# Optimization experiments

Measured on AMD Instinct MI355X. Metric: run time of the kernel, lower is better.

The kernel has to match this reference:

```python
import jax, jax.numpy as jnp
import numpy as np

EPS = 1e-6
N_HEADS = 16
N_KV_HEADS = 4
HEAD_DIM = 128
DIM = 2048
SEQ = 2048
BATCH = 2


def _make_freqs_cis(seqlen, head_dim, theta=10000.0):
    inv = 1.0 / (theta ** (jnp.arange(0, head_dim, 2, dtype=jnp.float32) / head_dim))  # [hd/2]
    t = jnp.arange(seqlen, dtype=jnp.float32)
    ang = jnp.outer(t, inv)  # [seq, hd/2]
    return jnp.stack([jnp.cos(ang), jnp.sin(ang)], axis=-1)  # [seq, hd/2, 2]


def setup_inputs() -> dict:
    key = jax.random.key(0)
    k1, k2, k3 = jax.random.split(key, 3)
    std = 0.02
    x = jax.random.normal(k1, (BATCH, SEQ, DIM), dtype=jnp.float32)
    freqs_cis = _make_freqs_cis(SEQ, HEAD_DIM)
    norm_w = jnp.ones((DIM,), dtype=jnp.float32)
    wqkv_w = jax.random.normal(k2, ((N_HEADS + 2 * N_KV_HEADS) * HEAD_DIM, DIM), dtype=jnp.float32) * std
    wo_w = jax.random.normal(k3, (DIM, N_HEADS * HEAD_DIM), dtype=jnp.float32) * std
    return {"x": x, "freqs_cis": freqs_cis, "norm_w": norm_w, "wqkv_w": wqkv_w, "wo_w": wo_w}


def _rope(t, cos, sin):
    # t: [b, s, h, hd] viewed as pairs; cos/sin: [s, hd/2]
    b, s, h, hd = t.shape
    tr = t.reshape(b, s, h, hd // 2, 2)
    xr, xi = tr[..., 0], tr[..., 1]
    c = cos[None, :, None, :]
    sn = sin[None, :, None, :]
    out_r = xr * c - xi * sn
    out_i = xr * sn + xi * c
    return jnp.stack([out_r, out_i], axis=-1).reshape(b, s, h, hd)


def reference(x, freqs_cis, norm_w, wqkv_w, wo_w):
    bs, seqlen, dim = x.shape
    n_rep = N_HEADS // N_KV_HEADS
    # RMSNorm
    xn = x * jax.lax.rsqrt(jnp.mean(x * x, axis=-1, keepdims=True) + EPS) * norm_w
    # fused QKV projection
    qkv = jnp.einsum('bsd,ed->bse', xn, wqkv_w)
    q_sz = N_HEADS * HEAD_DIM
    kv_sz = N_KV_HEADS * HEAD_DIM
    xq = qkv[..., :q_sz].reshape(bs, seqlen, N_HEADS, HEAD_DIM)
    xk = qkv[..., q_sz:q_sz + kv_sz].reshape(bs, seqlen, N_KV_HEADS, HEAD_DIM)
    xv = qkv[..., q_sz + kv_sz:].reshape(bs, seqlen, N_KV_HEADS, HEAD_DIM)
    cos, sin = freqs_cis[..., 0], freqs_cis[..., 1]
    xq = _rope(xq, cos, sin)
    xk = _rope(xk, cos, sin)
    # GQA: group q heads so kv broadcast replaces repeat_kv materialization
    q = xq.transpose(0, 2, 1, 3).reshape(bs, N_KV_HEADS, n_rep, seqlen, HEAD_DIM)
    k = xk.transpose(0, 2, 1, 3)  # [b, g, s, d]
    v = xv.transpose(0, 2, 1, 3)
    scale = 1.0 / jnp.sqrt(jnp.float32(HEAD_DIM))
    scores = jnp.einsum('bgrqd,bgkd->bgrqk', q, k) * scale
    causal = jnp.tril(jnp.ones((seqlen, seqlen), dtype=bool))
    scores = jnp.where(causal, scores, jnp.finfo(scores.dtype).min)
    probs = jax.nn.softmax(scores, axis=-1)
    out = jnp.einsum('bgrqk,bgkd->bgrqd', probs, v)
    out = out.reshape(bs, N_HEADS, seqlen, HEAD_DIM).transpose(0, 2, 1, 3).reshape(bs, seqlen, N_HEADS * HEAD_DIM)
    return jnp.einsum('bse,de->bsd', out, wo_w)
```

## Files before the change

### kernel.cpp

```cpp
#include <hip/hip_runtime.h>
#include <cstdint>
#include <cstddef>

typedef __bf16 bhalf;
typedef __bf16 bhalf8 __attribute__((ext_vector_type(8)));
typedef __bf16 bhalf4 __attribute__((ext_vector_type(4)));
typedef float f32x4 __attribute__((ext_vector_type(4)));
typedef float f32x16 __attribute__((ext_vector_type(16)));

#define RMS_EPS 1e-6f
#define N_HEADS 16
#define N_KV 4
#define HD 128
#define DIM 2048
#define SEQ 2048
#define BATCH 2

static __device__ __forceinline__ f32x4 mfma16(bhalf8 a, bhalf8 b, f32x4 c) {
    return __builtin_amdgcn_mfma_f32_16x16x32_bf16(a, b, c, 0, 0, 0);
}
static __device__ __forceinline__ f32x16 mfma32(bhalf8 a, bhalf8 b, f32x16 c) {
    return __builtin_amdgcn_mfma_f32_32x32x16_bf16(a, b, c, 0, 0, 0);
}

static __device__ __forceinline__ void gload16(const bhalf* g, bhalf* l) {
    __builtin_amdgcn_global_load_lds((const __attribute__((address_space(1))) unsigned int*)g,
                                     (__attribute__((address_space(3))) unsigned int*)l,
                                     16, 0, 0);
}

__global__ __launch_bounds__(256) void cvt_w(const float* __restrict__ a,
                                             const float* __restrict__ b,
                                             bhalf* __restrict__ dst) {
    size_t i = ((size_t)blockIdx.x * 256 + threadIdx.x) * 4;
    const size_t NQ = (size_t)3072 * 2048;
    float4 v = (i < NQ) ? ((const float4*)a)[i >> 2] : ((const float4*)b)[(i - NQ) >> 2];
    bhalf4 o;
    o[0] = (bhalf)v.x; o[1] = (bhalf)v.y; o[2] = (bhalf)v.z; o[3] = (bhalf)v.w;
    *(bhalf4*)(dst + i) = o;
}

__global__ __launch_bounds__(256) void rmsnorm_k(const float* __restrict__ x,
                                                 const float* __restrict__ w,
                                                 bhalf* __restrict__ xn) {
    const int row = blockIdx.x;
    const int tid = threadIdx.x;
    const float4* xr = (const float4*)(x + (size_t)row * DIM);
    float4 v0 = xr[tid * 2], v1 = xr[tid * 2 + 1];
    float ss = v0.x * v0.x + v0.y * v0.y + v0.z * v0.z + v0.w * v0.w
             + v1.x * v1.x + v1.y * v1.y + v1.z * v1.z + v1.w * v1.w;
    #pragma unroll
    for (int off = 32; off; off >>= 1) ss += __shfl_xor(ss, off, 64);
    __shared__ float red[4];
    if ((tid & 63) == 0) red[tid >> 6] = ss;
    __syncthreads();
    float tot = red[0] + red[1] + red[2] + red[3];
    float scale = rsqrtf(tot * (1.0f / DIM) + RMS_EPS);
    const float4* wr = (const float4*)w;
    float4 w0 = wr[tid * 2], w1 = wr[tid * 2 + 1];
    bhalf8 o;
    o[0] = (bhalf)(v0.x * scale * w0.x); o[1] = (bhalf)(v0.y * scale * w0.y);
    o[2] = (bhalf)(v0.z * scale * w0.z); o[3] = (bhalf)(v0.w * scale * w0.w);
    o[4] = (bhalf)(v1.x * scale * w1.x); o[5] = (bhalf)(v1.y * scale * w1.y);
    o[6] = (bhalf)(v1.z * scale * w1.z); o[7] = (bhalf)(v1.w * scale * w1.w);
    *(bhalf8*)(xn + (size_t)row * DIM + tid * 8) = o;
}

template <typename OutT>
__global__ __launch_bounds__(256) void gemm_abt(const bhalf* __restrict__ A,
                                                const bhalf* __restrict__ B,
                                                OutT* __restrict__ C,
                                                int N, int K) {
    const int tid = threadIdx.x;
    const int wave = tid >> 6, lane = tid & 63;
    const int quad = lane >> 4, r16 = lane & 15;
    const int m0 = blockIdx.y * 128, n0 = blockIdx.x * 128;
    const int wm = (wave >> 1) * 64, wn = (wave & 1) * 64;

    __shared__ __align__(16) bhalf sA[128][32];
    __shared__ __align__(16) bhalf sB[128][32];

    f32x4 acc[4][4];
    #pragma unroll
    for (int i = 0; i < 4; ++i)
        #pragma unroll
        for (int j = 0; j < 4; ++j) acc[i][j] = (f32x4)0.0f;

    const int lrow = lane >> 2;
    const int lcol = (lane & 3) * 8;
    const int arow = 32 * wave + lrow;
    const bhalf* Ap = A + (size_t)(m0 + arow) * K + lcol;
    const bhalf* Bp = B + (size_t)(n0 + arow) * K + lcol;
    const size_t rs16 = (size_t)16 * K;
    bhalf* sAp0 = &sA[32 * wave][0];
    bhalf* sAp1 = &sA[32 * wave + 16][0];
    bhalf* sBp0 = &sB[32 * wave][0];
    bhalf* sBp1 = &sB[32 * wave + 16][0];

    for (int k0 = 0; k0 < K; k0 += 32) {
        __syncthreads();
        gload16(Ap + k0, sAp0);
        gload16(Ap + k0 + rs16, sAp1);
        gload16(Bp + k0, sBp0);
        gload16(Bp + k0 + rs16, sBp1);
        __syncthreads();
        bhalf8 af[4], bfr[4];
        #pragma unroll
        for (int i = 0; i < 4; ++i) af[i]  = *(bhalf8*)&sA[wm + i * 16 + r16][quad * 8];
        #pragma unroll
        for (int j = 0; j < 4; ++j) bfr[j] = *(bhalf8*)&sB[wn + j * 16 + r16][quad * 8];
        #pragma unroll
        for (int i = 0; i < 4; ++i)
            #pragma unroll
            for (int j = 0; j < 4; ++j)
                acc[i][j] = mfma16(af[i], bfr[j], acc[i][j]);
    }

    #pragma unroll
    for (int i = 0; i < 4; ++i) {
        const int rbase = m0 + wm + i * 16 + quad * 4;
        #pragma unroll
        for (int rr = 0; rr < 4; ++rr) {
            OutT* crow = C + (size_t)(rbase + rr) * N + n0 + wn + r16;
            #pragma unroll
            for (int j = 0; j < 4; ++j) crow[j * 16] = (OutT)acc[i][j][rr];
        }
    }
}

__global__ __launch_bounds__(256) void rope_k(const bhalf* __restrict__ qkv,
                                              const float* __restrict__ freqs,
                                              bhalf* __restrict__ qb,
                                              bhalf* __restrict__ kb,
                                              bhalf* __restrict__ vt) {
    const int bs = blockIdx.x;
    const int b = bs >> 11, s = bs & 2047;
    const bhalf* row = qkv + (size_t)bs * 3072;
    const int tid = threadIdx.x;

    {
        const int h = tid >> 4, d20 = (tid & 15) * 4;
        bhalf8 e = *(const bhalf8*)(row + h * HD + d20 * 2);
        const float* fp = freqs + (size_t)s * 128 + d20 * 2;
        float4 f0 = *(const float4*)fp;
        float4 f1 = *(const float4*)(fp + 4);
        bhalf8 o;
        o[0] = (bhalf)((float)e[0] * f0.x - (float)e[1] * f0.y);
        o[1] = (bhalf)((float)e[0] * f0.y + (float)e[1] * f0.x);
        o[2] = (bhalf)((float)e[2] * f0.z - (float)e[3] * f0.w);
        o[3] = (bhalf)((float)e[2] * f0.w + (float)e[3] * f0.z);
        o[4] = (bhalf)((float)e[4] * f1.x - (float)e[5] * f1.y);
        o[5] = (bhalf)((float)e[4] * f1.y + (float)e[5] * f1.x);
        o[6] = (bhalf)((float)e[6] * f1.z - (float)e[7] * f1.w);
        o[7] = (bhalf)((float)e[6] * f1.w + (float)e[7] * f1.z);
        *(bhalf8*)(qb + ((size_t)(b * N_HEADS + h) * SEQ + s) * HD + d20 * 2) = o;
    }
    if (tid < 64) {
        const int kh = tid >> 4, d20 = (tid & 15) * 4;
        bhalf8 e = *(const bhalf8*)(row + 2048 + kh * HD + d20 * 2);
        const float* fp = freqs + (size_t)s * 128 + d20 * 2;
        float4 f0 = *(const float4*)fp;
        float4 f1 = *(const float4*)(fp + 4);
        bhalf8 o;
        o[0] = (bhalf)((float)e[0] * f0.x - (float)e[1] * f0.y);
        o[1] = (bhalf)((float)e[0] * f0.y + (float)e[1] * f0.x);
        o[2] = (bhalf)((float)e[2] * f0.z - (float)e[3] * f0.w);
        o[3] = (bhalf)((float)e[2] * f0.w + (float)e[3] * f0.z);
        o[4] = (bhalf)((float)e[4] * f1.x - (float)e[5] * f1.y);
        o[5] = (bhalf)((float)e[4] * f1.y + (float)e[5] * f1.x);
        o[6] = (bhalf)((float)e[6] * f1.z - (float)e[7] * f1.w);
        o[7] = (bhalf)((float)e[6] * f1.w + (float)e[7] * f1.z);
        *(bhalf8*)(kb + ((size_t)(b * N_KV + kh) * SEQ + s) * HD + d20 * 2) = o;
    }
    for (int e = tid; e < 512; e += 256) {
        const int kh = e >> 7, d = e & 127;
        vt[((size_t)(b * N_KV + kh) * HD + d) * SEQ + s] = row[2560 + e];
    }
}

__global__ __launch_bounds__(256, 1) void attn_k(const bhalf* __restrict__ qb,
                                                 const bhalf* __restrict__ kb,
                                                 const bhalf* __restrict__ vt,
                                                 bhalf* __restrict__ ob) {
    const int tid = threadIdx.x;
    const int wave = tid >> 6, lane = tid & 63;
    const int l31 = lane & 31, h2 = lane >> 5;
    const int pair = blockIdx.x & 7;
    const int hh = (blockIdx.x >> 3) & 15;
    const int b = blockIdx.x >> 7;
    const int kvh = hh >> 2;

    __shared__ __align__(16) bhalf sK[64][136];
    __shared__ __align__(16) bhalf sV[128][72];
    __shared__ __align__(16) bhalf sP[4][32][72];

    const bhalf* Kbase = kb + (size_t)(b * N_KV + kvh) * SEQ * HD;
    const bhalf* Vbase = vt + (size_t)(b * N_KV + kvh) * HD * SEQ;
    const float SCL2 = 0.08838834764831845f * 1.4426950408889634f;

    const int kr = tid >> 4, kc = (tid & 15) * 8;
    const int vr = tid >> 3, vc = (tid & 7) * 8;

    for (int phase = 0; phase < 2; ++phase) {
        const int qt = phase ? (15 - pair) : pair;
        const int ktmax = 2 * qt + 1;
        const int qrow = qt * 128 + wave * 32 + l31;

        const bhalf* qbase = qb + (((size_t)(b * N_HEADS + hh) * SEQ) + qrow) * HD;
        bhalf8 qf[8];
        #pragma unroll
        for (int kk = 0; kk < 8; ++kk) {
            bhalf8 q0 = *(const bhalf8*)(qbase + kk * 16 + h2 * 8);
            #pragma unroll
            for (int e = 0; e < 8; ++e) q0[e] = (bhalf)((float)q0[e] * SCL2);
            qf[kk] = q0;
        }

        f32x16 accO[4];
        #pragma unroll
        for (int dt = 0; dt < 4; ++dt) accO[dt] = (f32x16)0.0f;
        float m_i = -1e30f, l_i = 0.0f;

        bhalf8 kreg[4], vreg[4];
        #pragma unroll
        for (int i = 0; i < 4; ++i) {
            kreg[i] = *(const bhalf8*)(Kbase + (size_t)(kr + 16 * i) * HD + kc);
            vreg[i] = *(const bhalf8*)(Vbase + (size_t)(vr + 32 * i) * SEQ + vc);
        }

        for (int kt = 0; kt <= ktmax; ++kt) {
            __syncthreads();
            #pragma unroll
            for (int i = 0; i < 4; ++i) {
                *(bhalf8*)&sK[kr + 16 * i][kc] = kreg[i];
                *(bhalf8*)&sV[vr + 32 * i][vc] = vreg[i];
            }
            __syncthreads();
            if (kt < ktmax) {
                const int kn = (kt + 1) * 64;
                #pragma unroll
                for (int i = 0; i < 4; ++i) {
                    kreg[i] = *(const bhalf8*)(Kbase + (size_t)(kn + kr + 16 * i) * HD + kc);
                    vreg[i] = *(const bhalf8*)(Vbase + (size_t)(vr + 32 * i) * SEQ + kn + vc);
                }
            }

            if (qt * 128 + wave * 32 + 31 < kt * 64) continue;

            f32x16 accS[2];
            accS[0] = (f32x16)0.0f; accS[1] = (f32x16)0.0f;
            #pragma unroll
            for (int kk = 0; kk < 8; ++kk) {
                bhalf8 kf0 = *(bhalf8*)&sK[l31][kk * 16 + h2 * 8];
                bhalf8 kf1 = *(bhalf8*)&sK[32 + l31][kk * 16 + h2 * 8];
                accS[0] = mfma32(kf0, qf[kk], accS[0]);
                accS[1] = mfma32(kf1, qf[kk], accS[1]);
            }
            if (kt * 64 + 63 > qt * 128 + wave * 32) {
                #pragma unroll
                for (int nt = 0; nt < 2; ++nt)
                    #pragma unroll
                    for (int r = 0; r < 16; ++r) {
                        const int key = kt * 64 + nt * 32 + (r & 3) + 8 * (r >> 2) + 4 * h2;
                        if (key > qrow) accS[nt][r] = -1e30f;
                    }
            }

            float mx = -1e30f;
            #pragma unroll
            for (int nt = 0; nt < 2; ++nt)
                #pragma unroll
                for (int r = 0; r < 16; ++r) mx = fmaxf(mx, accS[nt][r]);
            mx = fmaxf(mx, __shfl_xor(mx, 32, 64));
            const float mnew = fmaxf(m_i, mx);
            const float alpha = exp2f(m_i - mnew);
            m_i = mnew;

            float rs = 0.0f;
            #pragma unroll
            for (int nt = 0; nt < 2; ++nt)
                #pragma unroll
                for (int c = 0; c < 4; ++c) {
                    bhalf4 pk;
                    #pragma unroll
                    for (int r = 0; r < 4; ++r) {
                        float p = exp2f(accS[nt][c * 4 + r] - mnew);
                        rs += p;
                        pk[r] = (bhalf)p;
                    }
                    *(bhalf4*)&sP[wave][l31][nt * 32 + c * 8 + h2 * 4] = pk;
                }
            rs += __shfl_xor(rs, 32, 64);
            l_i = l_i * alpha + rs;

            #pragma unroll
            for (int dt = 0; dt < 4; ++dt)
                #pragma unroll
                for (int r = 0; r < 16; ++r) accO[dt][r] *= alpha;

            #pragma unroll
            for (int kk2 = 0; kk2 < 4; ++kk2) {
                bhalf8 pf = *(bhalf8*)&sP[wave][l31][kk2 * 16 + h2 * 8];
                #pragma unroll
                for (int dt = 0; dt < 4; ++dt) {
                    bhalf8 vf = *(bhalf8*)&sV[dt * 32 + l31][kk2 * 16 + h2 * 8];
                    accO[dt] = mfma32(vf, pf, accO[dt]);
                }
            }
        }

        const float inv = 1.0f / l_i;
        bhalf* obase = ob + ((size_t)b * SEQ + qrow) * (size_t)(N_HEADS * HD) + hh * HD;
        #pragma unroll
        for (int dt = 0; dt < 4; ++dt)
            #pragma unroll
            for (int c = 0; c < 4; ++c) {
                bhalf4 o4;
                #pragma unroll
                for (int r = 0; r < 4; ++r) o4[r] = (bhalf)(accO[dt][c * 4 + r] * inv);
                *(bhalf4*)(obase + dt * 32 + c * 8 + h2 * 4) = o4;
            }
    }
}

extern "C" void kernel_launch(void* const* d_in, const int* in_sizes, int n_in,
                              void* d_out, int out_size, void* d_ws, size_t ws_size,
                              hipStream_t stream) {
    const float* x      = (const float*)d_in[0];
    const float* freqs  = (const float*)d_in[1];
    const float* norm_w = (const float*)d_in[2];
    const float* wqkv   = (const float*)d_in[3];
    const float* wo     = (const float*)d_in[4];
    float* out = (float*)d_out;

    char* ws = (char*)d_ws;
    bhalf* wqkv_b = (bhalf*)(ws);
    bhalf* wo_b   = (bhalf*)(ws + 12582912);
    bhalf* xn     = (bhalf*)(ws + 20971520);
    bhalf* qkv    = (bhalf*)(ws + 37748736);
    bhalf* qb     = (bhalf*)(ws + 88080384);
    bhalf* kb     = (bhalf*)(ws + 104857600);
    bhalf* vtb    = (bhalf*)(ws + 109051904);
    bhalf* attn   = (bhalf*)(ws + 113246208);

    cvt_w<<<10240, 256, 0, stream>>>(wqkv, wo, wqkv_b);
    rmsnorm_k<<<BATCH * SEQ, 256, 0, stream>>>(x, norm_w, xn);
    gemm_abt<bhalf><<<dim3(24, 32), 256, 0, stream>>>(xn, wqkv_b, qkv, 3072, 2048);
    rope_k<<<BATCH * SEQ, 256, 0, stream>>>(qkv, freqs, qb, kb, vtb);
    attn_k<<<256, 256, 0, stream>>>(qb, kb, vtb, attn);
    gemm_abt<float><<<dim3(16, 32), 256, 0, stream>>>(attn, wo_b, out, 2048, 2048);
}
```

Baseline: 336.0 us.

## Split attention KV tile across wave pairs and double the grid with merge

Attention blocks now cover 64 query rows instead of 128, doubling the grid to 512 blocks. Within a block, the four waves form two query groups and two key halves, and each wave handles a 32-key slice of every 64-key tile. The two key halves' partial softmax states are merged through shared memory at the end. Launch bounds allow two blocks per CU and exp2 uses the hardware intrinsic. The aim is more parallelism and occupancy and less causal-mask waste, at the cost of an extra merge pass with syncs and more per-block K/V tile loads.

```diff
diff --git a/kernel.cpp b/kernel.cpp
--- a/kernel.cpp
+++ b/kernel.cpp
@@ -178,21 +178,24 @@
     }
 }
 
-__global__ __launch_bounds__(256, 1) void attn_k(const bhalf* __restrict__ qb,
+__global__ __launch_bounds__(256, 2) void attn_k(const bhalf* __restrict__ qb,
                                                  const bhalf* __restrict__ kb,
                                                  const bhalf* __restrict__ vt,
                                                  bhalf* __restrict__ ob) {
     const int tid = threadIdx.x;
     const int wave = tid >> 6, lane = tid & 63;
     const int l31 = lane & 31, h2 = lane >> 5;
-    const int pair = blockIdx.x & 7;
-    const int hh = (blockIdx.x >> 3) & 15;
-    const int b = blockIdx.x >> 7;
+    const int qw = wave & 1, kw = wave >> 1;
+    const int pair = blockIdx.x & 15;
+    const int hh = (blockIdx.x >> 4) & 15;
+    const int b = blockIdx.x >> 8;
     const int kvh = hh >> 2;
 
-    __shared__ __align__(16) bhalf sK[64][136];
-    __shared__ __align__(16) bhalf sV[128][72];
-    __shared__ __align__(16) bhalf sP[4][32][72];
+    __shared__ __align__(16) bhalf smem[23040];
+    bhalf (*sK)[136] = (bhalf(*)[136])smem;
+    bhalf (*sV)[72]  = (bhalf(*)[72])(smem + 8704);
+    bhalf* sProw = smem + 17920 + (wave * 32 + l31) * 40;
+    float* mrg = (float*)smem;
 
     const bhalf* Kbase = kb + (size_t)(b * N_KV + kvh) * SEQ * HD;
     const bhalf* Vbase = vt + (size_t)(b * N_KV + kvh) * HD * SEQ;
@@ -200,11 +203,12 @@
 
     const int kr = tid >> 4, kc = (tid & 15) * 8;
     const int vr = tid >> 3, vc = (tid & 7) * 8;
+    const int mbase = (qw * 64 + lane) * 66;
 
     for (int phase = 0; phase < 2; ++phase) {
-        const int qt = phase ? (15 - pair) : pair;
-        const int ktmax = 2 * qt + 1;
-        const int qrow = qt * 128 + wave * 32 + l31;
+        const int qt = phase ? (31 - pair) : pair;
+        const int qrow = qt * 64 + qw * 32 + l31;
+        const int qhi = qt * 64 + qw * 32 + 31;
 
         const bhalf* qbase = qb + (((size_t)(b * N_HEADS + hh) * SEQ) + qrow) * HD;
         bhalf8 qf[8];
@@ -228,7 +232,7 @@
             vreg[i] = *(const bhalf8*)(Vbase + (size_t)(vr + 32 * i) * SEQ + vc);
         }
 
-        for (int kt = 0; kt <= ktmax; ++kt) {
+        for (int kt = 0; kt <= qt; ++kt) {
             __syncthreads();
             #pragma unroll
             for (int i = 0; i < 4; ++i) {
@@ -236,7 +240,7 @@
                 *(bhalf8*)&sV[vr + 32 * i][vc] = vreg[i];
             }
             __syncthreads();
-            if (kt < ktmax) {
+            if (kt < qt) {
                 const int kn = (kt + 1) * 64;
                 #pragma unroll
                 for (int i = 0; i < 4; ++i) {
@@ -244,52 +248,42 @@
                     vreg[i] = *(const bhalf8*)(Vbase + (size_t)(vr + 32 * i) * SEQ + kn + vc);
                 }
             }
-
-            if (qt * 128 + wave * 32 + 31 < kt * 64) continue;
-
-            f32x16 accS[2];
-            accS[0] = (f32x16)0.0f; accS[1] = (f32x16)0.0f;
-            #pragma unroll
-            for (int kk = 0; kk < 8; ++kk) {
-                bhalf8 kf0 = *(bhalf8*)&sK[l31][kk * 16 + h2 * 8];
-                bhalf8 kf1 = *(bhalf8*)&sK[32 + l31][kk * 16 + h2 * 8];
-                accS[0] = mfma32(kf0, qf[kk], accS[0]);
-                accS[1] = mfma32(kf1, qf[kk], accS[1]);
-            }
-            if (kt * 64 + 63 > qt * 128 + wave * 32) {
-                #pragma unroll
-                for (int nt = 0; nt < 2; ++nt)
-                    #pragma unroll
-                    for (int r = 0; r < 16; ++r) {
-                        const int key = kt * 64 + nt * 32 + (r & 3) + 8 * (r >> 2) + 4 * h2;
-                        if (key > qrow) accS[nt][r] = -1e30f;
-                    }
+            if (qhi < kt * 64 + kw * 32) continue;
+
+            f32x16 accS = (f32x16)0.0f;
+            const bhalf* kRow = &sK[kw * 32 + l31][0];
+            #pragma unroll
+            for (int kk = 0; kk < 8; ++kk)
+                accS = mfma32(*(bhalf8*)(kRow + kk * 16 + h2 * 8), qf[kk], accS);
+
+            if (kt == qt) {
+                #pragma unroll
+                for (int r = 0; r < 16; ++r) {
+                    const int key = kt * 64 + kw * 32 + (r & 3) + 8 * (r >> 2) + 4 * h2;
+                    if (key > qrow) accS[r] = -1e30f;
+                }
             }
 
             float mx = -1e30f;
             #pragma unroll
-            for (int nt = 0; nt < 2; ++nt)
-                #pragma unroll
-                for (int r = 0; r < 16; ++r) mx = fmaxf(mx, accS[nt][r]);
+            for (int r = 0; r < 16; ++r) mx = fmaxf(mx, accS[r]);
             mx = fmaxf(mx, __shfl_xor(mx, 32, 64));
             const float mnew = fmaxf(m_i, mx);
-            const float alpha = exp2f(m_i - mnew);
+            const float alpha = __builtin_amdgcn_exp2f(m_i - mnew);
             m_i = mnew;
 
             float rs = 0.0f;
             #pragma unroll
-            for (int nt = 0; nt < 2; ++nt)
-                #pragma unroll
-                for (int c = 0; c < 4; ++c) {
-                    bhalf4 pk;
-                    #pragma unroll
-                    for (int r = 0; r < 4; ++r) {
-                        float p = exp2f(accS[nt][c * 4 + r] - mnew);
-                        rs += p;
-                        pk[r] = (bhalf)p;
-                    }
-                    *(bhalf4*)&sP[wave][l31][nt * 32 + c * 8 + h2 * 4] = pk;
-                }
+            for (int c = 0; c < 4; ++c) {
+                bhalf4 pk;
+                #pragma unroll
+                for (int rr = 0; rr < 4; ++rr) {
+                    float p = __builtin_amdgcn_exp2f(accS[c * 4 + rr] - mnew);
+                    rs += p;
+                    pk[rr] = (bhalf)p;
+                }
+                *(bhalf4*)(sProw + c * 8 + h2 * 4) = pk;
+            }
             rs += __shfl_xor(rs, 32, 64);
             l_i = l_i * alpha + rs;
 
@@ -299,27 +293,48 @@
                 for (int r = 0; r < 16; ++r) accO[dt][r] *= alpha;
 
             #pragma unroll
-            for (int kk2 = 0; kk2 < 4; ++kk2) {
-                bhalf8 pf = *(bhalf8*)&sP[wave][l31][kk2 * 16 + h2 * 8];
+            for (int kk2 = 0; kk2 < 2; ++kk2) {
+                bhalf8 pf = *(bhalf8*)(sProw + kk2 * 16 + h2 * 8);
                 #pragma unroll
                 for (int dt = 0; dt < 4; ++dt) {
-                    bhalf8 vf = *(bhalf8*)&sV[dt * 32 + l31][kk2 * 16 + h2 * 8];
+                    bhalf8 vf = *(bhalf8*)&sV[dt * 32 + l31][kw * 32 + kk2 * 16 + h2 * 8];
                     accO[dt] = mfma32(vf, pf, accO[dt]);
                 }
             }
         }
 
-        const float inv = 1.0f / l_i;
-        bhalf* obase = ob + ((size_t)b * SEQ + qrow) * (size_t)(N_HEADS * HD) + hh * HD;
-        #pragma unroll
-        for (int dt = 0; dt < 4; ++dt)
-            #pragma unroll
-            for (int c = 0; c < 4; ++c) {
-                bhalf4 o4;
-                #pragma unroll
-                for (int r = 0; r < 4; ++r) o4[r] = (bhalf)(accO[dt][c * 4 + r] * inv);
-                *(bhalf4*)(obase + dt * 32 + c * 8 + h2 * 4) = o4;
-            }
+        __syncthreads();
+        if (kw == 1) {
+            #pragma unroll
+            for (int dt = 0; dt < 4; ++dt)
+                #pragma unroll
+                for (int r = 0; r < 16; ++r) mrg[mbase + dt * 16 + r] = accO[dt][r];
+            mrg[mbase + 64] = m_i;
+            mrg[mbase + 65] = l_i;
+        }
+        __syncthreads();
+        if (kw == 0) {
+            const float m1 = mrg[mbase + 64];
+            const float l1 = mrg[mbase + 65];
+            const float m = fmaxf(m_i, m1);
+            const float b0 = __builtin_amdgcn_exp2f(m_i - m);
+            const float b1 = __builtin_amdgcn_exp2f(m1 - m);
+            const float inv = 1.0f / (l_i * b0 + l1 * b1);
+            bhalf* obase = ob + ((size_t)b * SEQ + qrow) * (size_t)(N_HEADS * HD) + hh * HD;
+            #pragma unroll
+            for (int dt = 0; dt < 4; ++dt)
+                #pragma unroll
+                for (int c = 0; c < 4; ++c) {
+                    bhalf4 o4;
+                    #pragma unroll
+                    for (int rr = 0; rr < 4; ++rr) {
+                        const float v = accO[dt][c * 4 + rr] * b0 +
+                                        mrg[mbase + dt * 16 + c * 4 + rr] * b1;
+                        o4[rr] = (bhalf)(v * inv);
+                    }
+                    *(bhalf4*)(obase + dt * 32 + c * 8 + h2 * 4) = o4;
+                }
+        }
     }
 }
 
@@ -347,6 +362,6 @@
     rmsnorm_k<<<BATCH * SEQ, 256, 0, stream>>>(x, norm_w, xn);
     gemm_abt<bhalf><<<dim3(24, 32), 256, 0, stream>>>(xn, wqkv_b, qkv, 3072, 2048);
     rope_k<<<BATCH * SEQ, 256, 0, stream>>>(qkv, freqs, qb, kb, vtb);
-    attn_k<<<256, 256, 0, stream>>>(qb, kb, vtb, attn);
+    attn_k<<<512, 256, 0, stream>>>(qb, kb, vtb, attn);
     gemm_abt<float><<<dim3(16, 32), 256, 0, stream>>>(attn, wo_b, out, 2048, 2048);
 }
```

Result: faster. 319.4 us (-4.9%).
